# Optimization experiments

Measured on AMD Instinct MI355X. Metric: run time of the kernel, lower is better.

## Reference

```python
import jax, jax.numpy as jnp
import numpy as np

D_MODEL = 1024
N_HEADS = 16
D_K = D_MODEL // N_HEADS
SEQ = 4096
BATCH = 1
THETA = 10000.0


def setup_inputs() -> dict:
    key = jax.random.key(0)
    ks = jax.random.split(key, 5)
    scale = 0.02
    x = jax.random.normal(ks[0], (BATCH, SEQ, D_MODEL), dtype=jnp.float32)
    token_positions = jnp.broadcast_to(jnp.arange(SEQ, dtype=jnp.int64 if jax.config.jax_enable_x64 else jnp.int32)[None, :], (BATCH, SEQ))
    Wq = jax.random.normal(ks[1], (D_MODEL, D_MODEL), dtype=jnp.float32) * scale
    Wk = jax.random.normal(ks[2], (D_MODEL, D_MODEL), dtype=jnp.float32) * scale
    Wv = jax.random.normal(ks[3], (D_MODEL, D_MODEL), dtype=jnp.float32) * scale
    Wo = jax.random.normal(ks[4], (D_MODEL, D_MODEL), dtype=jnp.float32) * scale
    return {"x": x, "token_positions": token_positions, "Wq": Wq, "Wk": Wk, "Wv": Wv, "Wo": Wo}


def _apply_rope(t, token_positions, theta=THETA):
    # t: (b, h, s, d_k); token_positions: (b, s)
    d_k = t.shape[-1]
    inv_freq = theta ** (-jnp.arange(0, d_k, 2, dtype=jnp.float32) / d_k)  # (d_k/2,)
    ang = token_positions.astype(jnp.float32)[:, :, None] * inv_freq  # (b, s, d_k/2)
    cos = jnp.cos(ang)[:, None, :, :]  # (b, 1, s, d_k/2)
    sin = jnp.sin(ang)[:, None, :, :]
    te, to = t[..., 0::2], t[..., 1::2]
    re = te * cos - to * sin
    ro = te * sin + to * cos
    # interleave back: (..., d_k/2, 2) -> (..., d_k)
    return jnp.stack([re, ro], axis=-1).reshape(t.shape)


def reference(x, token_positions, Wq, Wk, Wv, Wo):
    b, s, d_model = x.shape
    h, d_k = N_HEADS, D_K
    q = (x @ Wq.T).reshape(b, s, h, d_k).transpose(0, 2, 1, 3)  # (b,h,s,d_k)
    k = (x @ Wk.T).reshape(b, s, h, d_k).transpose(0, 2, 1, 3)
    v = (x @ Wv.T).reshape(b, s, h, d_k).transpose(0, 2, 1, 3)
    q = _apply_rope(q, token_positions)
    k = _apply_rope(k, token_positions)
    scores = jnp.einsum('bhqd,bhkd->bhqk', q, k) / jnp.sqrt(jnp.float32(d_k))
    causal = jnp.tril(jnp.ones((s, s), dtype=bool))[None, None]
    scores = jnp.where(causal, scores, jnp.float32(-1e9))
    attn = jax.nn.softmax(scores, axis=-1)
    out = jnp.einsum('bhqk,bhkd->bhqd', attn, v)  # (b,h,s,d_k)
    out = out.transpose(0, 2, 1, 3).reshape(b, s, d_model)
    return out @ Wo.T
```

## Files before the change

kernel.cpp:

```cpp
#include <hip/hip_runtime.h>
#include <hip/hip_bf16.h>
#include <math.h>


#define SEQ 4096
#define DM  1024
#define NH  16
#define DK  64

typedef __attribute__((ext_vector_type(8))) short short8;
typedef __attribute__((ext_vector_type(4))) float floatx4;
typedef __attribute__((ext_vector_type(16))) float floatx16;
typedef __attribute__((ext_vector_type(4))) short short4v;

static __device__ __forceinline__ short f2bf(float f) {
    __hip_bfloat16 h = __float2bfloat16(f);
    return __builtin_bit_cast(short, h);
}

static __device__ __forceinline__ float fast_exp2(float x) {
#if __has_builtin(__builtin_amdgcn_exp2f)
    return __builtin_amdgcn_exp2f(x);
#else
    return exp2f(x);
#endif
}

static __device__ __forceinline__ short8 load8_f32_as_bf16(const float* p) {
    float4 a = *reinterpret_cast<const float4*>(p);
    float4 b = *reinterpret_cast<const float4*>(p + 4);
    short8 s;
    s[0] = f2bf(a.x); s[1] = f2bf(a.y); s[2] = f2bf(a.z); s[3] = f2bf(a.w);
    s[4] = f2bf(b.x); s[5] = f2bf(b.y); s[6] = f2bf(b.z); s[7] = f2bf(b.w);
    return s;
}

static __device__ __forceinline__ void gl2lds16(const __hip_bfloat16* g, short* l) {
    __builtin_amdgcn_global_load_lds(
        (const __attribute__((address_space(1))) unsigned int*)g,
        (__attribute__((address_space(3))) unsigned int*)l, 16, 0, 0);
}

static __device__ __forceinline__ int read_pos(const int* tp32, int s) {
    return (tp32[1] == 1) ? tp32[s] : tp32[2 * s];
}

__global__ __launch_bounds__(256) void prep_kernel(
    const float* __restrict__ x,  const float* __restrict__ Wq,
    const float* __restrict__ Wk, const float* __restrict__ Wv,
    const int* __restrict__ tp,
    __hip_bfloat16* __restrict__ xb,  __hip_bfloat16* __restrict__ Wqb,
    __hip_bfloat16* __restrict__ Wkb, __hip_bfloat16* __restrict__ Wvb,
    float2* __restrict__ tab)
{
    int b = blockIdx.x;
    if (b < 3584) {
        const float* src; __hip_bfloat16* dst; int off;
        if (b < 2048)      { src = x;  dst = xb;  off = b; }
        else if (b < 2560) { src = Wq; dst = Wqb; off = b - 2048; }
        else if (b < 3072) { src = Wk; dst = Wkb; off = b - 2560; }
        else               { src = Wv; dst = Wvb; off = b - 3072; }
        size_t i = (size_t)off * 256 + threadIdx.x;
        short8 v = load8_f32_as_bf16(src + i * 8);
        *reinterpret_cast<short8*>((short*)dst + i * 8) = v;
    } else {
        int idx = (b - 3584) * 256 + threadIdx.x;
        if (idx < SEQ * 32) {
            int s = idx >> 5, pair = idx & 31;
            float inv_freq = exp2f(-(float)(2 * pair) * (13.287712379549449f / 64.f));
            float sn, cs;
            sincosf((float)read_pos(tp, s) * inv_freq, &sn, &cs);
            tab[idx] = make_float2(cs, sn);
        }
    }
}

__global__ __launch_bounds__(256) void qkv_rope_kernel(
    const __hip_bfloat16* __restrict__ xb,
    const float2* __restrict__ tab,
    const __hip_bfloat16* __restrict__ Wqb,
    const __hip_bfloat16* __restrict__ Wkb,
    const __hip_bfloat16* __restrict__ Wvb,
    __hip_bfloat16* __restrict__ q_ws,
    __hip_bfloat16* __restrict__ k_ws,
    __hip_bfloat16* __restrict__ vt_ws)
{
    __shared__ __align__(16) short pool[17408];
    short* As = pool;
    short* Bs = pool + 8192;

    const int by = blockIdx.y;
    const int wsel = by >> 3;
    const __hip_bfloat16* W = (wsel == 0) ? Wqb : (wsel == 1 ? Wkb : Wvb);
    const int nloc0 = (by & 7) * 128;
    const int m0 = blockIdx.x * 128;

    const int t = threadIdx.x;
    const int lane = t & 63;
    const int w = t >> 6;
    const int quad = lane >> 4;
    const int ln = lane & 15;
    const int wm = (w >> 1) * 64;
    const int wn = (w & 1) * 64;

    floatx4 acc[4][4];
    #pragma unroll
    for (int i = 0; i < 4; i++)
        #pragma unroll
        for (int j = 0; j < 4; j++) acc[i][j] = (floatx4){0.f, 0.f, 0.f, 0.f};

    for (int k0 = 0; k0 < DM; k0 += 64) {
        #pragma unroll
        for (int it = 0; it < 4; it++) {
            int row = w * 32 + it * 8 + (lane >> 3);
            int sg = (lane & 7) ^ (row & 7);
            gl2lds16(&xb[(size_t)(m0 + row) * DM + k0 + sg * 8], &As[(w * 32 + it * 8) * 64]);
            gl2lds16(&W[(size_t)(nloc0 + row) * DM + k0 + sg * 8], &Bs[(w * 32 + it * 8) * 64]);
        }
        __syncthreads();

        short8 af[4][2], bfr[4][2];
        #pragma unroll
        for (int i = 0; i < 4; i++)
            #pragma unroll
            for (int kc = 0; kc < 2; kc++)
                af[i][kc] = *reinterpret_cast<const short8*>(
                    &As[(wm + i * 16 + ln) * 64 + (((kc * 4 + quad) ^ (ln & 7)) << 3)]);
        #pragma unroll
        for (int j = 0; j < 4; j++)
            #pragma unroll
            for (int kc = 0; kc < 2; kc++)
                bfr[j][kc] = *reinterpret_cast<const short8*>(
                    &Bs[(wn + j * 16 + ln) * 64 + (((kc * 4 + quad) ^ (ln & 7)) << 3)]);

        #pragma unroll
        for (int kc = 0; kc < 2; kc++)
            #pragma unroll
            for (int i = 0; i < 4; i++)
                #pragma unroll
                for (int j = 0; j < 4; j++)
                    acc[i][j] = __builtin_amdgcn_mfma_f32_16x16x32_bf16(
                        af[i][kc], bfr[j][kc], acc[i][j], 0, 0, 0);
        __syncthreads();
    }

    if (wsel < 2) {
        __hip_bfloat16* dst = (wsel == 0) ? q_ws : k_ws;
        const float qscale = (wsel == 0) ? 0.18033688011112042f : 1.0f;
        #pragma unroll
        for (int j = 0; j < 4; j++) {
            int cnl = wn + j * 16 + ln;
            int pair = ((nloc0 + cnl) & 63) >> 1;
            #pragma unroll
            for (int i = 0; i < 4; i++) {
                int rowl = wm + i * 16 + quad * 4;
                #pragma unroll
                for (int r = 0; r < 4; r++) {
                    float2 t2 = tab[(size_t)(m0 + rowl + r) * 32 + pair];
                    float val = acc[i][j][r];
                    float partner = __shfl_xor(val, 1, 64);
                    float res = val * t2.x + (((lane & 1) ? partner : -partner) * t2.y);
                    pool[(rowl + r) * 136 + cnl] = f2bf(res * qscale);
                }
            }
        }
        __syncthreads();
        int row = t >> 1, half = t & 1;
        size_t gbase = (size_t)(m0 + row) * DM + nloc0 + half * 64;
        #pragma unroll
        for (int c = 0; c < 8; c++)
            *reinterpret_cast<short8*>(&dst[gbase + c * 8]) =
                *reinterpret_cast<const short8*>(&pool[row * 136 + half * 64 + c * 8]);
    } else {
        #pragma unroll
        for (int j = 0; j < 4; j++) {
            int cnl = wn + j * 16 + ln;
            #pragma unroll
            for (int i = 0; i < 4; i++) {
                int s0 = wm + i * 16 + quad * 4;
                #pragma unroll
                for (int r = 0; r < 4; r++)
                    pool[cnl * 136 + s0 + r] = f2bf(acc[i][j][r]);
            }
        }
        __syncthreads();
        int cnl = t >> 1, sh = t & 1;
        size_t base = (size_t)(nloc0 + cnl) * SEQ + m0 + sh * 64;
        #pragma unroll
        for (int c = 0; c < 8; c++)
            *reinterpret_cast<short8*>(&vt_ws[base + c * 8]) =
                *reinterpret_cast<const short8*>(&pool[cnl * 136 + sh * 64 + c * 8]);
    }
}

__global__ __launch_bounds__(256, 2) void attn_kernel(
    const __hip_bfloat16* __restrict__ q_ws,
    const __hip_bfloat16* __restrict__ k_ws,
    const __hip_bfloat16* __restrict__ vt_ws,
    __hip_bfloat16* __restrict__ o_ws)
{
    __shared__ __align__(16) short Kt[2][128 * 64];
    __shared__ __align__(16) short Vt[2][64 * 128];

    const int bid = (int)blockIdx.x;
    const int head = bid & 15;
    const int jp = bid >> 4;

    const int t = threadIdx.x;
    const int lane = t & 63;
    const int w = t >> 6;
    const int hi = lane >> 5;
    const int l31 = lane & 31;

    auto stage = [&](int b, int kb) {
        #pragma unroll
        for (int i = 0; i < 4; i++) {
            int r = w * 32 + i * 8 + (lane >> 3);
            int keyloc = (r & ~12) | ((r & 4) << 1) | ((r & 8) >> 1);
            int g = (lane & 7) ^ (r & 7);
            gl2lds16(&k_ws[(size_t)(kb + keyloc) * DM + head * 64 + g * 8],
                     &Kt[b][(w * 32 + i * 8) * 64]);
        }
        #pragma unroll
        for (int i = 0; i < 4; i++) {
            int d = w * 16 + i * 4 + (lane >> 4);
            int g = (lane & 15) ^ (d & 7);
            gl2lds16(&vt_ws[(size_t)(head * 64 + d) * SEQ + kb + g * 8],
                     &Vt[b][(w * 16 + i * 4) * 128]);
        }
    };

    #pragma unroll 1
    for (int pass = 0; pass < 2; pass++) {
        const int tile = pass ? jp : (31 - jp);
        const int nstep = tile + 1;
        const int q0 = tile * 128 + w * 32;

        short8 qf[4];
        #pragma unroll
        for (int c = 0; c < 4; c++)
            qf[c] = *reinterpret_cast<const short8*>(
                &q_ws[(size_t)(q0 + l31) * DM + head * 64 + c * 16 + hi * 8]);

        floatx16 accO[2];
        #pragma unroll
        for (int db = 0; db < 2; db++)
            #pragma unroll
            for (int i = 0; i < 16; i++) accO[db][i] = 0.f;
        float l = 0.f;

        __syncthreads();
        stage(0, 0);
        int buf = 0;
        for (int st = 0; st < nstep; st++) {
            __syncthreads();
            if (st + 1 < nstep) stage(buf ^ 1, (st + 1) * 128);
            const bool last = (st == nstep - 1);

            #pragma unroll
            for (int kb32 = 0; kb32 < 4; kb32++) {
                if (!(last && kb32 > w)) {
                    const int krow = kb32 * 32 + l31;
                    short8 kfr[4];
                    #pragma unroll
                    for (int kc = 0; kc < 4; kc++) {
                        int g = (kc * 2 + hi) ^ (krow & 7);
                        kfr[kc] = *reinterpret_cast<const short8*>(&Kt[buf][krow * 64 + g * 8]);
                    }
                    floatx16 s;
                    #pragma unroll
                    for (int i = 0; i < 16; i++) s[i] = 0.f;
                    __builtin_amdgcn_s_setprio(1);
                    #pragma unroll
                    for (int kc = 0; kc < 4; kc++)
                        s = __builtin_amdgcn_mfma_f32_32x32x16_bf16(kfr[kc], qf[kc], s, 0, 0, 0);
                    __builtin_amdgcn_s_setprio(0);

                    if (last) {
                        #pragma unroll
                        for (int r = 0; r < 16; r++) {
                            int key_l = kb32 * 32 + (r & 7) + 2 * (r & 8) + 8 * hi;
                            if (key_l > w * 32 + l31) s[r] = -1e9f;
                        }
                    }
                    float p[16];
                    #pragma unroll
                    for (int r = 0; r < 16; r++) { p[r] = fast_exp2(s[r]); l += p[r]; }

                    union { short8 v; short e[8]; } pb[2];
                    #pragma unroll
                    for (int c = 0; c < 2; c++)
                        #pragma unroll
                        for (int e8 = 0; e8 < 8; e8++)
                            pb[c].e[e8] = f2bf(p[c * 8 + e8]);

                    #pragma unroll
                    for (int db = 0; db < 2; db++) {
                        const int vrow = db * 32 + l31;
                        short8 vfr[2];
                        #pragma unroll
                        for (int c = 0; c < 2; c++) {
                            int g = (kb32 * 4 + c * 2 + hi) ^ (vrow & 7);
                            vfr[c] = *reinterpret_cast<const short8*>(&Vt[buf][vrow * 128 + g * 8]);
                        }
                        __builtin_amdgcn_s_setprio(1);
                        accO[db] = __builtin_amdgcn_mfma_f32_32x32x16_bf16(vfr[0], pb[0].v, accO[db], 0, 0, 0);
                        accO[db] = __builtin_amdgcn_mfma_f32_32x32x16_bf16(vfr[1], pb[1].v, accO[db], 0, 0, 0);
                        __builtin_amdgcn_s_setprio(0);
                    }
                }
            }
            buf ^= 1;
        }

        float lf = l + __shfl_xor(l, 32, 64);
        float rl = 1.f / lf;

        __syncthreads();
        short* pool = (short*)Kt;
        const int qrow = w * 32 + l31;
        #pragma unroll
        for (int db = 0; db < 2; db++)
            #pragma unroll
            for (int j = 0; j < 4; j++) {
                union { short4v v; short e[4]; } g;
                #pragma unroll
                for (int m = 0; m < 4; m++)
                    g.e[m] = f2bf(accO[db][j * 4 + m] * rl);
                int dcol = db * 32 + j * 8 + 4 * hi;
                *reinterpret_cast<short4v*>(&pool[qrow * 68 + dcol]) = g.v;
            }
        __syncthreads();

        {
            int r = t >> 1, hh = t & 1;
            size_t gb = (size_t)(tile * 128 + r) * DM + head * 64 + hh * 32;
            #pragma unroll
            for (int c = 0; c < 2; c++) {
                union { short8 v8; short4v h[2]; } u;
                u.h[0] = *reinterpret_cast<const short4v*>(&pool[r * 68 + hh * 32 + c * 16]);
                u.h[1] = *reinterpret_cast<const short4v*>(&pool[r * 68 + hh * 32 + c * 16 + 4]);
                *reinterpret_cast<short8*>(&o_ws[gb + c * 16]) = u.v8;
                union { short8 v8; short4v h[2]; } u2;
                u2.h[0] = *reinterpret_cast<const short4v*>(&pool[r * 68 + hh * 32 + c * 16 + 8]);
                u2.h[1] = *reinterpret_cast<const short4v*>(&pool[r * 68 + hh * 32 + c * 16 + 12]);
                *reinterpret_cast<short8*>(&o_ws[gb + c * 16 + 8]) = u2.v8;
            }
        }
    }
}

__global__ __launch_bounds__(256) void oproj_kernel(
    const __hip_bfloat16* __restrict__ o_in,
    const float* __restrict__ Wo,
    float* __restrict__ out)
{
    __shared__ __align__(16) char smem[24576];
    short* As = (short*)smem;
    short* Bs = As + 8192;
    float* fpool = (float*)smem;

    const int m0 = blockIdx.x * 128;
    const int n0 = blockIdx.y * 64;

    const int t = threadIdx.x;
    const int lane = t & 63;
    const int w = t >> 6;
    const int quad = lane >> 4;
    const int ln = lane & 15;
    const int wm = (w >> 1) * 64;
    const int wn = (w & 1) * 32;

    floatx4 acc[4][2];
    #pragma unroll
    for (int i = 0; i < 4; i++)
        #pragma unroll
        for (int j = 0; j < 2; j++) acc[i][j] = (floatx4){0.f, 0.f, 0.f, 0.f};

    for (int k0 = 0; k0 < DM; k0 += 64) {
        #pragma unroll
        for (int it = 0; it < 4; it++) {
            int row = w * 32 + it * 8 + (lane >> 3);
            int sg = (lane & 7) ^ (row & 7);
            gl2lds16(&o_in[(size_t)(m0 + row) * DM + k0 + sg * 8], &As[(w * 32 + it * 8) * 64]);
        }
        #pragma unroll
        for (int p = 0; p < 2; p++) {
            int r = (t >> 3) + p * 32;
            int sg2 = t & 7;
            *reinterpret_cast<short8*>(&Bs[r * 64 + ((sg2 ^ (r & 7)) << 3)]) =
                load8_f32_as_bf16(&Wo[(size_t)(n0 + r) * DM + k0 + sg2 * 8]);
        }
        __syncthreads();

        short8 af[4][2], bfr[2][2];
        #pragma unroll
        for (int i = 0; i < 4; i++)
            #pragma unroll
            for (int kc = 0; kc < 2; kc++)
                af[i][kc] = *reinterpret_cast<const short8*>(
                    &As[(wm + i * 16 + ln) * 64 + (((kc * 4 + quad) ^ (ln & 7)) << 3)]);
        #pragma unroll
        for (int j = 0; j < 2; j++)
            #pragma unroll
            for (int kc = 0; kc < 2; kc++)
                bfr[j][kc] = *reinterpret_cast<const short8*>(
                    &Bs[(wn + j * 16 + ln) * 64 + (((kc * 4 + quad) ^ (ln & 7)) << 3)]);

        #pragma unroll
        for (int kc = 0; kc < 2; kc++)
            #pragma unroll
            for (int i = 0; i < 4; i++)
                #pragma unroll
                for (int j = 0; j < 2; j++)
                    acc[i][j] = __builtin_amdgcn_mfma_f32_16x16x32_bf16(
                        af[i][kc], bfr[j][kc], acc[i][j], 0, 0, 0);
        __syncthreads();
    }

    #pragma unroll
    for (int ph = 0; ph < 2; ph++) {
        if ((w >> 1) == ph) {
            #pragma unroll
            for (int j = 0; j < 2; j++)
                #pragma unroll
                for (int i = 0; i < 4; i++) {
                    int rl = i * 16 + quad * 4;
                    #pragma unroll
                    for (int r = 0; r < 4; r++)
                        fpool[(rl + r) * 68 + wn + j * 16 + ln] = acc[i][j][r];
                }
        }
        __syncthreads();
        int row = t >> 2;
        int c0 = (t & 3) * 16;
        size_t gbase = (size_t)(m0 + ph * 64 + row) * DM + n0 + c0;
        #pragma unroll
        for (int c = 0; c < 4; c++)
            *reinterpret_cast<float4*>(&out[gbase + c * 4]) =
                *reinterpret_cast<const float4*>(&fpool[row * 68 + c0 + c * 4]);
        __syncthreads();
    }
}

extern "C" void kernel_launch(void* const* d_in, const int* in_sizes, int n_in,
                              void* d_out, int out_size, void* d_ws, size_t ws_size,
                              hipStream_t stream) {
    const float* x  = (const float*)d_in[0];
    const int* tp   = (const int*)d_in[1];
    const float* Wq = (const float*)d_in[2];
    const float* Wk = (const float*)d_in[3];
    const float* Wv = (const float*)d_in[4];
    const float* Wo = (const float*)d_in[5];
    float* out = (float*)d_out;

    char* ws = (char*)d_ws;
    const size_t MB = 1024 * 1024;
    __hip_bfloat16* xb    = (__hip_bfloat16*)(ws);
    __hip_bfloat16* q_ws  = (__hip_bfloat16*)(ws + 8  * MB);
    __hip_bfloat16* k_ws  = (__hip_bfloat16*)(ws + 16 * MB);
    __hip_bfloat16* vt_ws = (__hip_bfloat16*)(ws + 24 * MB);
    __hip_bfloat16* o_ws  = xb;
    __hip_bfloat16* Wqb = (__hip_bfloat16*)d_out;
    __hip_bfloat16* Wkb = Wqb + (size_t)DM * DM;
    __hip_bfloat16* Wvb = Wkb + (size_t)DM * DM;
    float2* tab = (float2*)((char*)d_out + 6 * MB);

    prep_kernel<<<4096, 256, 0, stream>>>(x, Wq, Wk, Wv, tp, xb, Wqb, Wkb, Wvb, tab);
    qkv_rope_kernel<<<dim3(32, 24), 256, 0, stream>>>(xb, tab, Wqb, Wkb, Wvb, q_ws, k_ws, vt_ws);
    attn_kernel<<<256, 256, 0, stream>>>(q_ws, k_ws, vt_ws, o_ws);
    oproj_kernel<<<dim3(32, 16), 256, 0, stream>>>(o_ws, Wo, out);
}
```

Before: 222.9 us.

## Split attention key blocks across two wave groups with LDS reduction

The attention block grows from 256 to 512 threads. The second group of four waves processes the other half of each 128-key tile for the same 32 query rows, and the two partial O accumulators and row sums are merged through shared memory before normalisation. This doubles the waves per block to hide latency across 256 blocks on the GPU. In exchange it adds reduction traffic and extra barriers, halves per-wave staging, and lowers the allowed occupancy per CU.

```diff
diff --git a/kernel.cpp b/kernel.cpp
--- a/kernel.cpp
+++ b/kernel.cpp
@@ -193,7 +193,7 @@
     }
 }
 
-__global__ __launch_bounds__(256, 2) void attn_kernel(
+__global__ __launch_bounds__(512, 1) void attn_kernel(
     const __hip_bfloat16* __restrict__ q_ws,
     const __hip_bfloat16* __restrict__ k_ws,
     const __hip_bfloat16* __restrict__ vt_ws,
@@ -209,24 +209,26 @@
     const int t = threadIdx.x;
     const int lane = t & 63;
     const int w = t >> 6;
+    const int ww = w & 3;
+    const int kh = w >> 2;
     const int hi = lane >> 5;
     const int l31 = lane & 31;
 
     auto stage = [&](int b, int kb) {
         #pragma unroll
-        for (int i = 0; i < 4; i++) {
-            int r = w * 32 + i * 8 + (lane >> 3);
+        for (int i = 0; i < 2; i++) {
+            int r = w * 16 + i * 8 + (lane >> 3);
             int keyloc = (r & ~12) | ((r & 4) << 1) | ((r & 8) >> 1);
             int g = (lane & 7) ^ (r & 7);
             gl2lds16(&k_ws[(size_t)(kb + keyloc) * DM + head * 64 + g * 8],
-                     &Kt[b][(w * 32 + i * 8) * 64]);
-        }
-        #pragma unroll
-        for (int i = 0; i < 4; i++) {
-            int d = w * 16 + i * 4 + (lane >> 4);
+                     &Kt[b][(w * 16 + i * 8) * 64]);
+        }
+        #pragma unroll
+        for (int i = 0; i < 2; i++) {
+            int d = w * 8 + i * 4 + (lane >> 4);
             int g = (lane & 15) ^ (d & 7);
             gl2lds16(&vt_ws[(size_t)(head * 64 + d) * SEQ + kb + g * 8],
-                     &Vt[b][(w * 16 + i * 4) * 128]);
+                     &Vt[b][(w * 8 + i * 4) * 128]);
         }
     };
 
@@ -234,7 +236,7 @@
     for (int pass = 0; pass < 2; pass++) {
         const int tile = pass ? jp : (31 - jp);
         const int nstep = tile + 1;
-        const int q0 = tile * 128 + w * 32;
+        const int q0 = tile * 128 + ww * 32;
 
         short8 qf[4];
         #pragma unroll
@@ -258,8 +260,9 @@
             const bool last = (st == nstep - 1);
 
             #pragma unroll
-            for (int kb32 = 0; kb32 < 4; kb32++) {
-                if (!(last && kb32 > w)) {
+            for (int kk = 0; kk < 2; kk++) {
+                const int kb32 = kh * 2 + kk;
+                if (!(last && kb32 > ww)) {
                     const int krow = kb32 * 32 + l31;
                     short8 kfr[4];
                     #pragma unroll
@@ -280,7 +283,7 @@
                         #pragma unroll
                         for (int r = 0; r < 16; r++) {
                             int key_l = kb32 * 32 + (r & 7) + 2 * (r & 8) + 8 * hi;
-                            if (key_l > w * 32 + l31) s[r] = -1e9f;
+                            if (key_l > ww * 32 + l31) s[r] = -1e9f;
                         }
                     }
                     float p[16];
@@ -313,39 +316,62 @@
             buf ^= 1;
         }
 
+        float* xf = (float*)Vt;
+        const int xbase = (ww * 64 + lane) * 19;
+        __syncthreads();
+        if (kh == 1) {
+            #pragma unroll
+            for (int i = 0; i < 16; i++) xf[xbase + i] = accO[0][i];
+            xf[xbase + 16] = l;
+        }
+        __syncthreads();
+        if (kh == 0) {
+            #pragma unroll
+            for (int i = 0; i < 16; i++) accO[0][i] += xf[xbase + i];
+            l += xf[xbase + 16];
+        }
+        __syncthreads();
+        if (kh == 1) {
+            #pragma unroll
+            for (int i = 0; i < 16; i++) xf[xbase + i] = accO[1][i];
+        }
+        __syncthreads();
+        if (kh == 0) {
+            #pragma unroll
+            for (int i = 0; i < 16; i++) accO[1][i] += xf[xbase + i];
+        }
+
         float lf = l + __shfl_xor(l, 32, 64);
         float rl = 1.f / lf;
 
-        __syncthreads();
         short* pool = (short*)Kt;
-        const int qrow = w * 32 + l31;
-        #pragma unroll
-        for (int db = 0; db < 2; db++)
-            #pragma unroll
-            for (int j = 0; j < 4; j++) {
-                union { short4v v; short e[4]; } g;
-                #pragma unroll
-                for (int m = 0; m < 4; m++)
-                    g.e[m] = f2bf(accO[db][j * 4 + m] * rl);
-                int dcol = db * 32 + j * 8 + 4 * hi;
-                *reinterpret_cast<short4v*>(&pool[qrow * 68 + dcol]) = g.v;
-            }
+        if (kh == 0) {
+            const int qrow = ww * 32 + l31;
+            #pragma unroll
+            for (int db = 0; db < 2; db++)
+                #pragma unroll
+                for (int j = 0; j < 4; j++) {
+                    union { short4v v; short e[4]; } g;
+                    #pragma unroll
+                    for (int m = 0; m < 4; m++)
+                        g.e[m] = f2bf(accO[db][j * 4 + m] * rl);
+                    int dcol = db * 32 + j * 8 + 4 * hi;
+                    *reinterpret_cast<short4v*>(&pool[qrow * 68 + dcol]) = g.v;
+                }
+        }
         __syncthreads();
 
         {
-            int r = t >> 1, hh = t & 1;
-            size_t gb = (size_t)(tile * 128 + r) * DM + head * 64 + hh * 32;
-            #pragma unroll
-            for (int c = 0; c < 2; c++) {
-                union { short8 v8; short4v h[2]; } u;
-                u.h[0] = *reinterpret_cast<const short4v*>(&pool[r * 68 + hh * 32 + c * 16]);
-                u.h[1] = *reinterpret_cast<const short4v*>(&pool[r * 68 + hh * 32 + c * 16 + 4]);
-                *reinterpret_cast<short8*>(&o_ws[gb + c * 16]) = u.v8;
-                union { short8 v8; short4v h[2]; } u2;
-                u2.h[0] = *reinterpret_cast<const short4v*>(&pool[r * 68 + hh * 32 + c * 16 + 8]);
-                u2.h[1] = *reinterpret_cast<const short4v*>(&pool[r * 68 + hh * 32 + c * 16 + 12]);
-                *reinterpret_cast<short8*>(&o_ws[gb + c * 16 + 8]) = u2.v8;
-            }
+            int r = t >> 2, q4 = t & 3;
+            size_t gb = (size_t)(tile * 128 + r) * DM + head * 64 + q4 * 16;
+            union { short8 v8; short4v h[2]; } u;
+            u.h[0] = *reinterpret_cast<const short4v*>(&pool[r * 68 + q4 * 16]);
+            u.h[1] = *reinterpret_cast<const short4v*>(&pool[r * 68 + q4 * 16 + 4]);
+            *reinterpret_cast<short8*>(&o_ws[gb]) = u.v8;
+            union { short8 v8; short4v h[2]; } u2;
+            u2.h[0] = *reinterpret_cast<const short4v*>(&pool[r * 68 + q4 * 16 + 8]);
+            u2.h[1] = *reinterpret_cast<const short4v*>(&pool[r * 68 + q4 * 16 + 12]);
+            *reinterpret_cast<short8*>(&o_ws[gb + 8]) = u2.v8;
         }
     }
 }
@@ -468,6 +494,6 @@
 
     prep_kernel<<<4096, 256, 0, stream>>>(x, Wq, Wk, Wv, tp, xb, Wqb, Wkb, Wvb, tab);
     qkv_rope_kernel<<<dim3(32, 24), 256, 0, stream>>>(xb, tab, Wqb, Wkb, Wvb, q_ws, k_ws, vt_ws);
-    attn_kernel<<<256, 256, 0, stream>>>(q_ws, k_ws, vt_ws, o_ws);
+    attn_kernel<<<256, 512, 0, stream>>>(q_ws, k_ws, vt_ws, o_ws);
     oproj_kernel<<<dim3(32, 16), 256, 0, stream>>>(o_ws, Wo, out);
 }
```

Result: faster. 210.4 us (-5.6%).
